# Kernel optimization log

Hardware: AMD Instinct MI355X
Metric: run time of the kernel (lower is better)

Reference implementation:

```python
import jax, jax.numpy as jnp
import numpy as np

N_HEADS, N_LEVELS, N_POINTS, D_MODEL = 8, 3, 12, 64
PARAM_NAMES = ['vp0_w','vp0_b','vp1_w','vp1_b','so0_w','so0_b','so1_w','so1_b','so2_w','so2_b','so3_w','so3_b','aw0_w','aw0_b','aw1_w','aw1_b','aw2_w','aw2_b','aw3_w','aw3_b','op0_w','op0_b','op1_w','op1_b']

def _lrelu(x):
    return jnp.where(x >= 0, x, 0.1 * x)

def _conv(x, w, b):
    y = jax.lax.conv_general_dilated(x, w, (1, 1), 'SAME', dimension_numbers=('NCHW', 'OIHW', 'NCHW'))
    return y + b[None, :, None, None]

def _bilinear(img, px, py):
    # img [B,C,H,W]; px,py [B,Q] absolute pixel coords; zero padding (grid_sample 'zeros')
    B, C, H, W = img.shape
    flat = img.reshape(B, C, H * W)
    x0 = jnp.floor(px); y0 = jnp.floor(py)
    wx1 = px - x0; wy1 = py - y0
    def g(xi, yi, wgt):
        valid = (xi >= 0) & (xi <= W - 1) & (yi >= 0) & (yi <= H - 1)
        xi_c = jnp.clip(xi, 0, W - 1).astype(jnp.int32)
        yi_c = jnp.clip(yi, 0, H - 1).astype(jnp.int32)
        v = jnp.take_along_axis(flat, (yi_c * W + xi_c)[:, None, :], axis=2)
        return v * (wgt * valid)[:, None, :]
    return (g(x0, y0, (1 - wx1) * (1 - wy1)) + g(x0 + 1, y0, wx1 * (1 - wy1))
          + g(x0, y0 + 1, (1 - wx1) * wy1) + g(x0 + 1, y0 + 1, wx1 * wy1))

def _flow_warp(img, flow):
    # img [n,C,h,w]; flow [n,2,h,w] (x,y); matches grid_sample align_corners=True
    n, C, h, w = img.shape
    gy, gx = jnp.meshgrid(jnp.arange(h, dtype=img.dtype), jnp.arange(w, dtype=img.dtype), indexing='ij')
    px = (gx[None] + flow[:, 0]).reshape(n, h * w)
    py = (gy[None] + flow[:, 1]).reshape(n, h * w)
    return _bilinear(img, px, py).reshape(n, C, h, w)

def _forward(x, flow_1, flow_2, flip_flow_1, flip_flow_2, p):
    n, t, c, h, w = x.shape
    hw = h * w; THW = t * hw
    M, L, P, D = N_HEADS, N_LEVELS, N_POINTS, c // N_HEADS
    flow_cn1 = flow_1
    flow_cn2 = flow_1 + _flow_warp(flow_2, flow_1)
    flow_n1c, flow_n1n2 = flip_flow_1, flow_2
    flow_n2n1 = flip_flow_2
    flow_n2c = flip_flow_2 + _flow_warp(flip_flow_1, flip_flow_2)
    warp_cn1 = _flow_warp(x[:, 1], flow_cn1)
    warp_cn2 = _flow_warp(x[:, 2], flow_cn2)
    warp_n1c = _flow_warp(x[:, 0], flow_n1c)
    warp_n1n2 = _flow_warp(x[:, 2], flow_n1n2)
    warp_n2n1 = _flow_warp(x[:, 1], flow_n2n1)
    warp_n2c = _flow_warp(x[:, 0], flow_n2c)
    extra = jnp.concatenate([x[:, 0], warp_cn1, warp_cn2, warp_n1c, warp_n1n2, warp_n2n1, warp_n2c,
                             flow_cn1, flow_cn2, flow_n1c, flow_n1n2, flow_n2n1, flow_n2c], axis=1)
    value = _conv(_lrelu(_conv(x.reshape(n, t * c, h, w), p['vp0_w'], p['vp0_b'])), p['vp1_w'], p['vp1_b'])
    def head(e, pre):
        y = _lrelu(_conv(e, p[pre + '0_w'], p[pre + '0_b']))
        y = _lrelu(_conv(y, p[pre + '1_w'], p[pre + '1_b']))
        y = _lrelu(_conv(y, p[pre + '2_w'], p[pre + '2_b']))
        return _conv(y, p[pre + '3_w'], p[pre + '3_b'])
    so = head(extra, 'so')  # [n, L*M*L*P*2, h, w]
    aw = head(extra, 'aw')  # [n, L*M*L*P*9, h, w]
    so = so.reshape(n, t, -1, hw).transpose(0, 1, 3, 2).reshape(n, THW, M, L, P, 2)
    aw = aw.reshape(n, t, -1, hw).transpose(0, 1, 3, 2).reshape(n, THW, M, L * P * 9)
    aw = jax.nn.softmax(aw, axis=-1).reshape(n, THW, M, L, P * 9)
    # flow-guided offsets: add per-(query-frame, target-level) flow to learned offsets
    off = so.reshape(n, t, hw, M, L, P, 2)
    fz = jnp.zeros_like(flow_cn2)
    def lvl(f0, f1, f2):
        s = jnp.stack([f0, f1, f2], 1)  # [n,3,2,h,w]
        return s.transpose(0, 3, 4, 1, 2).reshape(n, hw, L, 2)[:, None, :, None, :, None, :]
    off = jnp.concatenate([
        off[:, 0:1] + lvl(fz, flow_cn1, flow_cn2),
        off[:, 1:2] + lvl(flow_n1c, fz, flow_n1n2),
        off[:, 2:3] + lvl(flow_n2c, flow_n2n1, fz)], axis=1).reshape(n, THW, M, L, P, 2)
    # 3x3 integer patch around each sampling point
    pi, pj = jnp.meshgrid(jnp.arange(-1, 2), jnp.arange(-1, 2), indexing='ij')
    patch = jnp.stack([pi, pj], -1).reshape(1, 1, 1, 1, 1, 9, 2).astype(off.dtype)
    off = (off[..., None, :] + patch).reshape(n, THW, M, L, P * 9, 2)
    # reference points (valid_ratios are all 1: full masks are zeros)
    ry, rx = jnp.meshgrid((jnp.arange(h) + 0.5) / h, (jnp.arange(w) + 0.5) / w, indexing='ij')
    ref = jnp.stack([rx, ry], -1).reshape(1, hw, 2).astype(off.dtype)
    ref = jnp.tile(ref, (1, t, 1))  # [1, THW, 2]
    norm = jnp.array([w, h], dtype=off.dtype)
    loc = ref[:, :, None, None, None, :] + off / norm  # [n,THW,M,L,P*9,2] normalized
    # multi-scale deformable attention (all L levels share (h,w)); align_corners=False, zeros pad
    P9 = P * 9
    v = value.reshape(n, t, c, hw).transpose(0, 1, 3, 2).reshape(n, THW, M, D)
    vl = v.reshape(n, L, hw, M, D).transpose(0, 3, 1, 4, 2).reshape(n * M * L, D, h, w)
    px = (loc[..., 0] * w - 0.5).transpose(0, 2, 3, 1, 4).reshape(n * M * L, THW * P9)
    py = (loc[..., 1] * h - 0.5).transpose(0, 2, 3, 1, 4).reshape(n * M * L, THW * P9)
    sampled = _bilinear(vl, px, py).reshape(n, M, L, D, THW, P9)
    out = jnp.einsum('nmldqp,nqmlp->nqmd', sampled, aw).reshape(n, THW, c)
    out = out.reshape(n, t, h, w, c).transpose(0, 1, 4, 2, 3).reshape(n, t * c, h, w)
    out = _conv(_lrelu(_conv(out, p['op0_w'], p['op0_b'])), p['op1_w'], p['op1_b'])
    return out.reshape(n, t, c, h, w) + x

def setup_inputs():
    key = jax.random.key(0)
    n, t, c, h, w = 1, 3, 64, 32, 32
    ks = jax.random.split(key, 24)
    d = {}
    d['x'] = jax.random.normal(ks[0], (n, t, c, h, w), jnp.float32)
    for i, name in enumerate(['flow_1', 'flow_2', 'flip_flow_1', 'flip_flow_2']):
        d[name] = jax.random.normal(ks[1 + i], (n, 2, h, w), jnp.float32)
    cin_extra = 7 * c + 12
    specs = [('vp0', t * c, t * c), ('vp1', t * c, t * c),
             ('so0', c, cin_extra), ('so1', c, c), ('so2', c, c), ('so3', N_LEVELS * N_HEADS * N_LEVELS * N_POINTS * 2, c),
             ('aw0', c, cin_extra), ('aw1', c, c), ('aw2', c, c), ('aw3', N_LEVELS * N_HEADS * N_LEVELS * N_POINTS * 9, c),
             ('op0', t * c, t * c), ('op1', t * c, t * c)]
    for i, (name, co, ci) in enumerate(specs):
        kw, kb = jax.random.split(ks[5 + i])
        std = (2.0 / (ci * 9)) ** 0.5
        d[name + '_w'] = jax.random.normal(kw, (co, ci, 3, 3), jnp.float32) * std
        d[name + '_b'] = jax.random.normal(kb, (co,), jnp.float32) * 0.01
    return d

def reference(x, flow_1, flow_2, flip_flow_1, flip_flow_2, vp0_w, vp0_b, vp1_w, vp1_b, so0_w, so0_b, so1_w, so1_b, so2_w, so2_b, so3_w, so3_b, aw0_w, aw0_b, aw1_w, aw1_b, aw2_w, aw2_b, aw3_w, aw3_b, op0_w, op0_b, op1_w, op1_b):
    p = dict(zip(PARAM_NAMES, (vp0_w, vp0_b, vp1_w, vp1_b, so0_w, so0_b, so1_w, so1_b, so2_w, so2_b, so3_w, so3_b, aw0_w, aw0_b, aw1_w, aw1_b, aw2_w, aw2_b, aw3_w, aw3_b, op0_w, op0_b, op1_w, op1_b)))
    return _forward(x, flow_1, flow_2, flip_flow_1, flip_flow_2, p)
```

## Files before the change

### kernel.cpp

```cpp
#include <hip/hip_runtime.h>
#include <math.h>

#define HW 1024

typedef __attribute__((ext_vector_type(8))) short bf16x8;
typedef __attribute__((ext_vector_type(4))) float floatx4;

__device__ __forceinline__ unsigned short f2bf(float f) {
    unsigned u = __float_as_uint(f);
    u += 0x7FFF + ((u >> 16) & 1);
    return (unsigned short)(u >> 16);
}
__device__ __forceinline__ float bf2f(unsigned short u) {
    return __uint_as_float(((unsigned)u) << 16);
}
__device__ __forceinline__ float bflo(unsigned u) { return __uint_as_float(u << 16); }
__device__ __forceinline__ float bfhi(unsigned u) { return __uint_as_float(u & 0xffff0000u); }

__device__ __forceinline__ float bilin32(const float* __restrict__ img, float px, float py) {
    float x0f = floorf(px), y0f = floorf(py);
    float wx = px - x0f, wy = py - y0f;
    bool vx0 = (x0f >= 0.f) && (x0f <= 31.f);
    bool vx1 = (x0f >= -1.f) && (x0f <= 30.f);
    bool vy0 = (y0f >= 0.f) && (y0f <= 31.f);
    bool vy1 = (y0f >= -1.f) && (y0f <= 30.f);
    int ix0 = (int)fminf(fmaxf(x0f, 0.f), 31.f);
    int iy0 = (int)fminf(fmaxf(y0f, 0.f), 31.f);
    int ix1 = (int)fminf(fmaxf(x0f + 1.f, 0.f), 31.f);
    int iy1 = (int)fminf(fmaxf(y0f + 1.f, 0.f), 31.f);
    float w00 = (1.f - wx) * (1.f - wy) * ((vx0 && vy0) ? 1.f : 0.f);
    float w01 = wx * (1.f - wy) * ((vx1 && vy0) ? 1.f : 0.f);
    float w10 = (1.f - wx) * wy * ((vx0 && vy1) ? 1.f : 0.f);
    float w11 = wx * wy * ((vx1 && vy1) ? 1.f : 0.f);
    return w00 * img[iy0 * 32 + ix0] + w01 * img[iy0 * 32 + ix1] +
           w10 * img[iy1 * 32 + ix0] + w11 * img[iy1 * 32 + ix1];
}

__device__ __forceinline__ float2 comp_flow(const float* __restrict__ fa,
                                            const float* __restrict__ fb, int pix) {
    int y = pix >> 5, x = pix & 31;
    float fx = fa[pix], fy = fa[HW + pix];
    float px = (float)x + fx, py = (float)y + fy;
    float2 r;
    r.x = fx + bilin32(fb, px, py);
    r.y = fy + bilin32(fb + HW, px, py);
    return r;
}

struct WD { const float* src; int cout, Cin, nCb, wbase, beg; };
struct PrepP {
    const float *x, *f1, *f2, *ff1, *ff2;
    float *fcn2, *fn2c;
    unsigned short *x_pad, *extra_pad, *wgt;
    WD wd[12];
};

__global__ __launch_bounds__(256) void prep_k(PrepP P) {
    __shared__ float wlds[16 * 288];
    const int b = blockIdx.x, tid = threadIdx.x;
    if (b < 192) {
        int idx = b * 256 + tid;
        int pix = idx / 48, c4 = idx - pix * 48;
        int y = pix >> 5, xx = pix & 31;
        int c0 = c4 * 4;
        ushort4 s;
        s.x = f2bf(P.x[(size_t)(c0 + 0) * HW + pix]);
        s.y = f2bf(P.x[(size_t)(c0 + 1) * HW + pix]);
        s.z = f2bf(P.x[(size_t)(c0 + 2) * HW + pix]);
        s.w = f2bf(P.x[(size_t)(c0 + 3) * HW + pix]);
        *(ushort4*)(&P.x_pad[(size_t)((y + 1) * 34 + xx + 1) * 192 + c0]) = s;
    } else if (b < 2112) {
        int idx = (b - 192) * 256 + tid;
        int ch = idx >> 10, pix = idx & 1023;
        int y = pix >> 5, xx = pix & 31;
        float v = 0.f;
        if (ch < 64) {
            v = P.x[(size_t)ch * HW + pix];
        } else if (ch < 448) {
            int grp = (ch - 64) >> 6;
            int c = (ch - 64) & 63;
            const float* src;
            float fx, fy;
            if (grp == 0)      { src = P.x + 64 * HW;  fx = P.f1[pix];  fy = P.f1[HW + pix]; }
            else if (grp == 1) { src = P.x + 128 * HW; float2 r = comp_flow(P.f1, P.f2, pix);  fx = r.x; fy = r.y; }
            else if (grp == 2) { src = P.x;            fx = P.ff1[pix]; fy = P.ff1[HW + pix]; }
            else if (grp == 3) { src = P.x + 128 * HW; fx = P.f2[pix];  fy = P.f2[HW + pix]; }
            else if (grp == 4) { src = P.x + 64 * HW;  fx = P.ff2[pix]; fy = P.ff2[HW + pix]; }
            else               { src = P.x;            float2 r = comp_flow(P.ff2, P.ff1, pix); fx = r.x; fy = r.y; }
            v = bilin32(src + c * HW, (float)xx + fx, (float)y + fy);
        } else if (ch < 460) {
            int fc = ch - 448;
            int which = fc >> 1, comp = fc & 1;
            if (which == 0)      v = P.f1[comp * HW + pix];
            else if (which == 1) { float2 r = comp_flow(P.f1, P.f2, pix);  v = comp ? r.y : r.x; }
            else if (which == 2) v = P.ff1[comp * HW + pix];
            else if (which == 3) v = P.f2[comp * HW + pix];
            else if (which == 4) v = P.ff2[comp * HW + pix];
            else                 { float2 r = comp_flow(P.ff2, P.ff1, pix); v = comp ? r.y : r.x; }
        }
        P.extra_pad[(size_t)((y + 1) * 34 + xx + 1) * 480 + ch] = f2bf(v);
    } else if (b < 2128) {
        int idx = (b - 2112) * 256 + tid;
        if (idx < 1024) {
            float2 r = comp_flow(P.f1, P.f2, idx);
            P.fcn2[idx] = r.x; P.fcn2[HW + idx] = r.y;
        } else if (idx < 2048) {
            int pix = idx - 1024;
            float2 r = comp_flow(P.ff2, P.ff1, pix);
            P.fn2c[pix] = r.x; P.fn2c[HW + pix] = r.y;
        }
    } else if (b < 2144) {
        const int chans[9] = {192, 192, 480, 64, 64, 64, 64, 192, 192};
        size_t offs[9]; size_t a = 0;
        for (int i = 0; i < 9; ++i) { offs[i] = a; a += (size_t)1156 * chans[i]; }
        int bb = b - 2128;
        for (int item = bb; item < 9 * 132; item += 16) {
            int buf = item / 132, i = item - buf * 132;
            int py, px;
            if (i < 34) { py = 0; px = i; }
            else if (i < 68) { py = 33; px = i - 34; }
            else { int j = i - 68; py = 1 + (j >> 1); px = (j & 1) ? 33 : 0; }
            int C = chans[buf];
            unsigned short* p = P.x_pad + offs[buf] + (size_t)(py * 34 + px) * C;
            for (int c = tid; c < C; c += 256) p[c] = 0;
        }
    } else {
        int blk = b - 2144;
        int di = 0;
        while (di < 11 && blk >= P.wd[di + 1].beg) ++di;
        WD w = P.wd[di];
        int local = blk - w.beg;
        int co16 = local / w.nCb, cb = local - co16 * w.nCb;
        int cr0 = co16 * 16, ci0 = cb * 32;
        for (int i = tid; i < 16 * 288; i += 256) {
            int cr = i / 288, o = i - cr * 288;
            int crg = cr0 + cr, ci = ci0 + o / 9;
            float v = (crg < w.cout && ci < w.Cin)
                ? w.src[((size_t)crg * w.Cin + ci0) * 9 + o] : 0.f;
            wlds[i] = v;
        }
        __syncthreads();
        for (int e = tid; e < 9 * 512; e += 256) {
            int t = e >> 9, idx = e & 511;
            int j = idx & 7, lane = idx >> 3, q = lane >> 4, mm = lane & 15;
            P.wgt[((size_t)w.wbase + ((size_t)co16 * 9 + t) * w.nCb + cb) * 512 + idx] =
                f2bf(wlds[mm * 288 + (q * 8 + j) * 9 + t]);
        }
    }
}

struct CDesc {
    const unsigned short* in;
    const unsigned short* wgt;
    const float* bias;
    void* out;
    const float* residual;
    int Cpad, nCb, Cout, mode, cmod, relu, Mblocks;
};
struct CParam { CDesc d[4]; };

template<int PIXROWS, int COBLK>
__global__ __launch_bounds__(256) void conv_mfma_k(CParam P) {
    constexpr int TROWS = PIXROWS + 2;
    constexpr int TC = TROWS * 34 * 4;
    constexpr int ITRIPS = (TC + 255) / 256;
    constexpr int NTY = PIXROWS / 4;
    constexpr int NACC = NTY * 2;
    constexpr int MT = COBLK / 16;
    constexpr int WN = MT * 9 * 64;
    constexpr int WTRIPS = (WN + 255) / 256;
    __shared__ unsigned short blds[TROWS * 34 * 40];
    __shared__ unsigned short wlds[MT * 9 * 512];

    int bx = blockIdx.x;
    int di = 0;
    while (bx >= P.d[di].Mblocks) { bx -= P.d[di].Mblocks; ++di; }
    const CDesc d = P.d[di];

    const int tid = threadIdx.x;
    const int w = tid >> 6, lane = tid & 63;
    const int lq = lane >> 4, ln = lane & 15;
    const int co0 = bx * COBLK;
    const int by = blockIdx.y, y0 = by * PIXROWS;
    const unsigned short* __restrict__ in = d.in;
    const unsigned short* __restrict__ wg = d.wgt;
    const int Cpad = d.Cpad, nCb = d.nCb;

    floatx4 acc[MT][NACC];
#pragma unroll
    for (int mt = 0; mt < MT; ++mt)
#pragma unroll
        for (int nt = 0; nt < NACC; ++nt)
            acc[mt][nt] = (floatx4){0.f, 0.f, 0.f, 0.f};

    bf16x8 ireg[ITRIPS];
    bf16x8 wreg[WTRIPS];

    auto load_regs = [&](int cb) {
        const int ci0 = cb << 5;
#pragma unroll
        for (int k = 0; k < ITRIPS; ++k) {
            int i = tid + k * 256;
            if (i < TC) {
                int r = i / 136, rem = i - r * 136, c = rem >> 2, g = rem & 3;
                ireg[k] = *(const bf16x8*)(in + (size_t)((y0 + r) * 34 + c) * Cpad + ci0 + g * 8);
            }
        }
#pragma unroll
        for (int k = 0; k < WTRIPS; ++k) {
            int i = tid + k * 256;
            if (i < WN) {
                int chunk = i >> 6, l16 = i & 63;
                int mt = chunk / 9, t = chunk - mt * 9;
                wreg[k] = *(const bf16x8*)(wg + ((size_t)(((co0 >> 4) + mt) * 9 + t) * nCb + cb) * 512 + l16 * 8);
            }
        }
    };

    load_regs(0);

    for (int cb = 0; cb < nCb; ++cb) {
        __syncthreads();
#pragma unroll
        for (int k = 0; k < ITRIPS; ++k) {
            int i = tid + k * 256;
            if (i < TC) {
                int r = i / 136, rem = i - r * 136, c = rem >> 2, g = rem & 3;
                *(bf16x8*)(&blds[(r * 34 + c) * 40 + g * 8]) = ireg[k];
            }
        }
#pragma unroll
        for (int k = 0; k < WTRIPS; ++k) {
            int i = tid + k * 256;
            if (i < WN) {
                int chunk = i >> 6, l16 = i & 63;
                *(bf16x8*)(&wlds[chunk * 512 + l16 * 8]) = wreg[k];
            }
        }
        __syncthreads();
        if (cb + 1 < nCb) load_regs(cb + 1);
        for (int t = 0; t < 9; ++t) {
            const int dy = t / 3, dx = t - dy * 3;
            bf16x8 bfr[NACC];
#pragma unroll
            for (int ty = 0; ty < NTY; ++ty)
#pragma unroll
                for (int tx = 0; tx < 2; ++tx) {
                    int yy = w * NTY + ty + dy;
                    int xx = tx * 16 + ln + dx;
                    bfr[ty * 2 + tx] = *(const bf16x8*)(&blds[(yy * 34 + xx) * 40 + lq * 8]);
                }
#pragma unroll
            for (int mt = 0; mt < MT; ++mt) {
                bf16x8 afr = *(const bf16x8*)(&wlds[(mt * 9 + t) * 512 + lane * 8]);
#pragma unroll
                for (int nt = 0; nt < NACC; ++nt)
                    acc[mt][nt] = __builtin_amdgcn_mfma_f32_16x16x32_bf16(afr, bfr[nt], acc[mt][nt], 0, 0, 0);
            }
        }
    }

#pragma unroll
    for (int mt = 0; mt < MT; ++mt) {
        const int co = co0 + mt * 16 + lq * 4;
        if (co >= d.Cout) continue;
        float bv[4];
#pragma unroll
        for (int r = 0; r < 4; ++r) bv[r] = d.bias[co + r];
#pragma unroll
        for (int nt = 0; nt < NACC; ++nt) {
            const int ty = nt >> 1, tx = nt & 1;
            const int pix = by * (PIXROWS * 32) + (w * NTY + ty) * 32 + tx * 16 + ln;
            float v[4];
#pragma unroll
            for (int r = 0; r < 4; ++r) {
                float vv = acc[mt][nt][r] + bv[r];
                if (d.relu) vv = (vv >= 0.f) ? vv : 0.1f * vv;
                v[r] = vv;
            }
            if (d.mode == 0) {
                float* o = (float*)d.out;
#pragma unroll
                for (int r = 0; r < 4; ++r) {
                    float vv = v[r];
                    if (d.residual) vv += d.residual[(size_t)(co + r) * HW + pix];
                    o[(size_t)(co + r) * HW + pix] = vv;
                }
            } else if (d.mode == 1) {
                int fq = co / d.cmod, cc = co - fq * d.cmod;
                *(float4*)((float*)d.out + ((size_t)fq * HW + pix) * d.cmod + cc) =
                    make_float4(v[0], v[1], v[2], v[3]);
            } else if (d.mode == 2) {
                int fq = co / d.cmod, cc = co - fq * d.cmod;
                ushort4 s4;
                s4.x = f2bf(v[0]); s4.y = f2bf(v[1]); s4.z = f2bf(v[2]); s4.w = f2bf(v[3]);
                *(ushort4*)((unsigned short*)d.out + ((size_t)fq * HW + pix) * d.cmod + cc) = s4;
            } else {
                int yy = (pix >> 5) + 1, xx = (pix & 31) + 1;
                ushort4 s4;
                s4.x = f2bf(v[0]); s4.y = f2bf(v[1]); s4.z = f2bf(v[2]); s4.w = f2bf(v[3]);
                *(ushort4*)((unsigned short*)d.out + (size_t)(yy * 34 + xx) * d.cmod + co) = s4;
            }
        }
    }
}

__global__ __launch_bounds__(256) void deform_attn_k(
    const unsigned short* __restrict__ value_b, const float* __restrict__ so_t,
    const unsigned short* __restrict__ aw_t,
    const float* __restrict__ flow_1, const float* __restrict__ flow_2,
    const float* __restrict__ flip_flow_1, const float* __restrict__ flip_flow_2,
    const float* __restrict__ flow_cn2, const float* __restrict__ flow_n2c,
    unsigned short* __restrict__ attn_pad)
{
    __shared__ unsigned short vlds[24576];
    __shared__ unsigned short pwlds[4][432];
    const int tid = threadIdx.x;
    const int wav = tid >> 6, lane = tid & 63;
    const int m = blockIdx.x & 7, qc = blockIdx.x >> 3;

    for (int i = tid; i < 3072; i += 256) {
        int l = i >> 10, p = i & 1023;
        *(bf16x8*)(&vlds[(size_t)i * 8]) =
            *(const bf16x8*)(value_b + ((size_t)((l * 8 + m) * 1024) + p) * 8);
    }
    __syncthreads();

    const int pp = lane & 15, gq = lane >> 4;
    const int gdy = (gq >> 1) * 2 - 1;
    const int gdx = (gq & 1) * 2 - 1;
    const bool selx = (gq & 1);
    const bool sely = (gq >> 1);

    for (int r = 0; r < 8; ++r) {
        const int q = qc * 32 + r * 4 + wav;
        const int f = q >> 10, pix = q & 1023;
        const int y = pix >> 5, x = pix & 31;

        float flx0 = 0.f, fly0 = 0.f, flx1 = 0.f, fly1 = 0.f, flx2 = 0.f, fly2 = 0.f;
        if (f == 0) {
            flx1 = flow_1[pix];      fly1 = flow_1[HW + pix];
            flx2 = flow_cn2[pix];    fly2 = flow_cn2[HW + pix];
        } else if (f == 1) {
            flx0 = flip_flow_1[pix]; fly0 = flip_flow_1[HW + pix];
            flx2 = flow_2[pix];      fly2 = flow_2[HW + pix];
        } else {
            flx0 = flow_n2c[pix];    fly0 = flow_n2c[HW + pix];
            flx1 = flip_flow_2[pix]; fly1 = flip_flow_2[HW + pix];
        }

        const unsigned short* awp = aw_t + (size_t)q * 2592 + m * 324;
        float av[6];
        float vmax = -1e30f;
#pragma unroll
        for (int it = 0; it < 6; ++it) {
            int j = lane + it * 64;
            float a = (j < 324) ? bf2f(awp[j]) : -1e30f;
            av[it] = a;
            vmax = fmaxf(vmax, a);
        }
#pragma unroll
        for (int off = 32; off; off >>= 1) vmax = fmaxf(vmax, __shfl_xor(vmax, off));
        float ssum = 0.f;
#pragma unroll
        for (int it = 0; it < 6; ++it) {
            int j = lane + it * 64;
            float e = (j < 324) ? __expf(av[it] - vmax) : 0.f;
            av[it] = e;
            ssum += e;
        }
#pragma unroll
        for (int off = 32; off; off >>= 1) ssum += __shfl_xor(ssum, off);
        const float inv = 1.f / ssum;

#pragma unroll
        for (int it = 0; it < 6; ++it) {
            int j = lane + it * 64;
            if (j < 324) {
                int pi = j / 9, k = j - pi * 9;
                pwlds[wav][pi * 12 + k] = f2bf(av[it] * inv);
            }
        }

        float acc[8];
#pragma unroll
        for (int dd = 0; dd < 8; ++dd) acc[dd] = 0.f;
        const float* sop = so_t + (size_t)q * 576 + m * 72;

#pragma unroll
        for (int pt = 0; pt < 3; ++pt) {
            int pi = pt * 16 + pp;
            if (pi < 36) {
                int l = pi / 12;
                float2 so2 = *(const float2*)(sop + pi * 2);
                float fx = (l == 0) ? flx0 : (l == 1) ? flx1 : flx2;
                float fy = (l == 0) ? fly0 : (l == 1) ? fly1 : fly2;
                float bxf = (float)x + so2.x + fx;
                float byf = (float)y + so2.y + fy;
                float x0f = floorf(bxf), y0f = floorf(byf);
                float wx = bxf - x0f, wy = byf - y0f;
                float ax = 1.f - wx, ay = 1.f - wy;
                int x0 = (int)fminf(fmaxf(x0f, -2.f), 34.f);
                int y0 = (int)fminf(fmaxf(y0f, -2.f), 34.f);

                const unsigned short* pr = &pwlds[wav][pi * 12];
                uint2 pv0 = *(const uint2*)(pr);
                uint2 pv1 = *(const uint2*)(pr + 4);
                float a0 = bflo(pv0.x), a1 = bfhi(pv0.x), a2 = bflo(pv0.y);
                float a3 = bfhi(pv0.y), a4 = bflo(pv1.x), a5 = bfhi(pv1.x);
                float a6 = bflo(pv1.y), a7 = bfhi(pv1.y), a8 = bf2f(pr[8]);

                float bs0a, bs0b, bs1a, bs1b, bs2a, bs2b;
                {
                    float b0, b1, b2, b3;
                    b0 = a0 * ax; b1 = a0 * wx + a3 * ax; b2 = a3 * wx + a6 * ax; b3 = a6 * wx;
                    bs0a = selx ? b2 : b0; bs0b = selx ? b3 : b1;
                    b0 = a1 * ax; b1 = a1 * wx + a4 * ax; b2 = a4 * wx + a7 * ax; b3 = a7 * wx;
                    bs1a = selx ? b2 : b0; bs1b = selx ? b3 : b1;
                    b0 = a2 * ax; b1 = a2 * wx + a5 * ax; b2 = a5 * wx + a8 * ax; b3 = a8 * wx;
                    bs2a = selx ? b2 : b0; bs2b = selx ? b3 : b1;
                }
                float c00, c01, c10, c11;
                {
                    float c0 = bs0a * ay, c1 = bs0a * wy + bs1a * ay;
                    float c2 = bs1a * wy + bs2a * ay, c3 = bs2a * wy;
                    c00 = sely ? c2 : c0; c10 = sely ? c3 : c1;
                    c0 = bs0b * ay; c1 = bs0b * wy + bs1b * ay;
                    c2 = bs1b * wy + bs2b * ay; c3 = bs2b * wy;
                    c01 = sely ? c2 : c0; c11 = sely ? c3 : c1;
                }
                float cg[2][2] = {{c00, c01}, {c10, c11}};
                const int vbase = l * 1024;
#pragma unroll
                for (int sy = 0; sy < 2; ++sy) {
#pragma unroll
                    for (int sx = 0; sx < 2; ++sx) {
                        int dy = gdy + sy, dx = gdx + sx;
                        float pyf = y0f + (float)dy, pxf = x0f + (float)dx;
                        bool v = (pxf >= 0.f) && (pxf <= 31.f) && (pyf >= 0.f) && (pyf <= 31.f);
                        int px = min(max(x0 + dx, 0), 31);
                        int py = min(max(y0 + dy, 0), 31);
                        float c = cg[sy][sx] * (v ? 1.f : 0.f);
                        uint4 vv = *(const uint4*)(&vlds[(size_t)(vbase + py * 32 + px) * 8]);
                        acc[0] = fmaf(c, bflo(vv.x), acc[0]);
                        acc[1] = fmaf(c, bfhi(vv.x), acc[1]);
                        acc[2] = fmaf(c, bflo(vv.y), acc[2]);
                        acc[3] = fmaf(c, bfhi(vv.y), acc[3]);
                        acc[4] = fmaf(c, bflo(vv.z), acc[4]);
                        acc[5] = fmaf(c, bfhi(vv.z), acc[5]);
                        acc[6] = fmaf(c, bflo(vv.w), acc[6]);
                        acc[7] = fmaf(c, bfhi(vv.w), acc[7]);
                    }
                }
            }
        }

#pragma unroll
        for (int dd = 0; dd < 8; ++dd) {
#pragma unroll
            for (int off = 32; off; off >>= 1) acc[dd] += __shfl_xor(acc[dd], off);
        }
        if (lane == 0) {
            unsigned short* op = attn_pad + (size_t)((y + 1) * 34 + x + 1) * 192 + f * 64 + m * 8;
            ushort4 s0, s1;
            s0.x = f2bf(acc[0]); s0.y = f2bf(acc[1]); s0.z = f2bf(acc[2]); s0.w = f2bf(acc[3]);
            s1.x = f2bf(acc[4]); s1.y = f2bf(acc[5]); s1.z = f2bf(acc[6]); s1.w = f2bf(acc[7]);
            *(ushort4*)(op) = s0;
            *(ushort4*)(op + 4) = s1;
        }
    }
}

extern "C" void kernel_launch(void* const* d_in, const int* in_sizes, int n_in,
                              void* d_out, int out_size, void* d_ws, size_t ws_size,
                              hipStream_t stream) {
    const float* x      = (const float*)d_in[0];
    const float* flow_1 = (const float*)d_in[1];
    const float* flow_2 = (const float*)d_in[2];
    const float* flip_1 = (const float*)d_in[3];
    const float* flip_2 = (const float*)d_in[4];
    const float* vp0_w = (const float*)d_in[5];  const float* vp0_b = (const float*)d_in[6];
    const float* vp1_w = (const float*)d_in[7];  const float* vp1_b = (const float*)d_in[8];
    const float* so0_w = (const float*)d_in[9];  const float* so0_b = (const float*)d_in[10];
    const float* so1_w = (const float*)d_in[11]; const float* so1_b = (const float*)d_in[12];
    const float* so2_w = (const float*)d_in[13]; const float* so2_b = (const float*)d_in[14];
    const float* so3_w = (const float*)d_in[15]; const float* so3_b = (const float*)d_in[16];
    const float* aw0_w = (const float*)d_in[17]; const float* aw0_b = (const float*)d_in[18];
    const float* aw1_w = (const float*)d_in[19]; const float* aw1_b = (const float*)d_in[20];
    const float* aw2_w = (const float*)d_in[21]; const float* aw2_b = (const float*)d_in[22];
    const float* aw3_w = (const float*)d_in[23]; const float* aw3_b = (const float*)d_in[24];
    const float* op0_w = (const float*)d_in[25]; const float* op0_b = (const float*)d_in[26];
    const float* op1_w = (const float*)d_in[27]; const float* op1_b = (const float*)d_in[28];
    float* out = (float*)d_out;
    (void)ws_size; (void)in_sizes; (void)n_in; (void)out_size;

    float* fws = (float*)d_ws;
    float* flow_cn2 = fws;
    float* flow_n2c = flow_cn2 + 2048;
    unsigned short* value_b = (unsigned short*)(flow_n2c + 2048);
    float* so_t     = (float*)(value_b + 196608);
    unsigned short* uws = (unsigned short*)(so_t + 1769472);
    unsigned short* x_pad     = uws;
    unsigned short* vp0h      = x_pad + 1156 * 192;
    unsigned short* extra_pad = vp0h + 1156 * 192;
    unsigned short* s1 = extra_pad + 1156 * 480;
    unsigned short* a1 = s1 + 1156 * 64;
    unsigned short* s2 = a1 + 1156 * 64;
    unsigned short* a2 = s2 + 1156 * 64;
    unsigned short* attn_pad = a2 + 1156 * 64;
    unsigned short* op0h     = attn_pad + 1156 * 192;
    unsigned short* aw_t = op0h + 1156 * 192;
    unsigned short* wgt  = aw_t + (size_t)3072 * 2592;

    PrepP pp;
    pp.x = x; pp.f1 = flow_1; pp.f2 = flow_2; pp.ff1 = flip_1; pp.ff2 = flip_2;
    pp.fcn2 = flow_cn2; pp.fn2c = flow_n2c;
    pp.x_pad = x_pad; pp.extra_pad = extra_pad; pp.wgt = wgt;
    pp.wd[0]  = {vp0_w, 192, 192, 6,     0,    0};
    pp.wd[1]  = {vp1_w, 192, 192, 6,   648,   72};
    pp.wd[2]  = {so0_w,  64, 460, 15, 1296,  144};
    pp.wd[3]  = {aw0_w,  64, 460, 15, 1836,  204};
    pp.wd[4]  = {so1_w,  64,  64, 2,  2376,  264};
    pp.wd[5]  = {aw1_w,  64,  64, 2,  2448,  272};
    pp.wd[6]  = {so2_w,  64,  64, 2,  2520,  280};
    pp.wd[7]  = {aw2_w,  64,  64, 2,  2592,  288};
    pp.wd[8]  = {so3_w, 1728, 64, 2,  2664,  296};
    pp.wd[9]  = {aw3_w, 7776, 64, 2,  4608,  512};
    pp.wd[10] = {op0_w, 192, 192, 6, 13392, 1488};
    pp.wd[11] = {op1_w, 192, 192, 6, 14040, 1560};
    prep_k<<<3776, 256, 0, stream>>>(pp);

    const int BIG = 1 << 30;
    CDesc nul = {nullptr, nullptr, nullptr, nullptr, nullptr, 0, 0, 0, 0, 0, 0, BIG};

    {
        CParam cp;
        cp.d[0] = {x_pad,     wgt + (size_t)0 * 512,    vp0_b, vp0h, nullptr, 192, 6,  192, 3, 192, 1, 12};
        cp.d[1] = {extra_pad, wgt + (size_t)1296 * 512, so0_b, s1,   nullptr, 480, 15, 64,  3, 64,  1, 4};
        cp.d[2] = {extra_pad, wgt + (size_t)1836 * 512, aw0_b, a1,   nullptr, 480, 15, 64,  3, 64,  1, 4};
        cp.d[3] = nul;
        conv_mfma_k<4, 16><<<dim3(20, 8), 256, 0, stream>>>(cp);
    }
    {
        CParam cp;
        cp.d[0] = {vp0h, wgt + (size_t)648 * 512,  vp1_b, value_b, nullptr, 192, 6, 192, 2, 8,  0, 12};
        cp.d[1] = {s1,   wgt + (size_t)2376 * 512, so1_b, s2,      nullptr, 64,  2, 64,  3, 64, 1, 4};
        cp.d[2] = {a1,   wgt + (size_t)2448 * 512, aw1_b, a2,      nullptr, 64,  2, 64,  3, 64, 1, 4};
        cp.d[3] = nul;
        conv_mfma_k<4, 16><<<dim3(20, 8), 256, 0, stream>>>(cp);
    }
    {
        CParam cp;
        cp.d[0] = {s2, wgt + (size_t)2520 * 512, so2_b, s1, nullptr, 64, 2, 64, 3, 64, 1, 4};
        cp.d[1] = {a2, wgt + (size_t)2592 * 512, aw2_b, a1, nullptr, 64, 2, 64, 3, 64, 1, 4};
        cp.d[2] = nul; cp.d[3] = nul;
        conv_mfma_k<4, 16><<<dim3(8, 8), 256, 0, stream>>>(cp);
    }
    {
        CParam cp;
        cp.d[0] = {s1, wgt + (size_t)2664 * 512, so3_b, so_t, nullptr, 64, 2, 1728, 1, 576,  0, 27};
        cp.d[1] = {a1, wgt + (size_t)4608 * 512, aw3_b, aw_t, nullptr, 64, 2, 7776, 2, 2592, 0, 122};
        cp.d[2] = nul; cp.d[3] = nul;
        conv_mfma_k<8, 64><<<dim3(149, 4), 256, 0, stream>>>(cp);
    }

    deform_attn_k<<<768, 256, 0, stream>>>(value_b, so_t, aw_t,
                                           flow_1, flow_2, flip_1, flip_2,
                                           flow_cn2, flow_n2c, attn_pad);

    {
        CParam cp;
        cp.d[0] = {attn_pad, wgt + (size_t)13392 * 512, op0_b, op0h, nullptr, 192, 6, 192, 3, 192, 1, 12};
        cp.d[1] = nul; cp.d[2] = nul; cp.d[3] = nul;
        conv_mfma_k<4, 16><<<dim3(12, 8), 256, 0, stream>>>(cp);
    }
    {
        CParam cp;
        cp.d[0] = {op0h, wgt + (size_t)14040 * 512, op1_b, out, x, 192, 6, 192, 0, 0, 0, 12};
        cp.d[1] = nul; cp.d[2] = nul; cp.d[3] = nul;
        conv_mfma_k<4, 16><<<dim3(12, 8), 256, 0, stream>>>(cp);
    }
}
```

Before: 269.9 us.

## Spread weight transforms across conv launches and vectorize extra-channel prep

```diff
diff --git a/kernel.cpp b/kernel.cpp
--- a/kernel.cpp
+++ b/kernel.cpp
@@ -48,15 +48,38 @@
 }
 
 struct WD { const float* src; int cout, Cin, nCb, wbase, beg; };
+
+__device__ __forceinline__ void wxform_tile(const WD w, int local,
+                                            unsigned short* __restrict__ wgt, char* smraw) {
+    float* wlds = (float*)smraw;
+    const int tid = threadIdx.x;
+    int co16 = local / w.nCb, cb = local - co16 * w.nCb;
+    int cr0 = co16 * 16, ci0 = cb * 32;
+    for (int i = tid; i < 16 * 288; i += 256) {
+        int cr = i / 288, o = i - cr * 288;
+        int crg = cr0 + cr, ci = ci0 + o / 9;
+        float v = (crg < w.cout && ci < w.Cin)
+            ? w.src[((size_t)crg * w.Cin + ci0) * 9 + o] : 0.f;
+        wlds[i] = v;
+    }
+    __syncthreads();
+    for (int e = tid; e < 9 * 512; e += 256) {
+        int t = e >> 9, idx = e & 511;
+        int j = idx & 7, lane = idx >> 3, q = lane >> 4, mm = lane & 15;
+        wgt[((size_t)w.wbase + ((size_t)co16 * 9 + t) * w.nCb + cb) * 512 + idx] =
+            f2bf(wlds[mm * 288 + (q * 8 + j) * 9 + t]);
+    }
+}
+
 struct PrepP {
     const float *x, *f1, *f2, *ff1, *ff2;
     float *fcn2, *fn2c;
     unsigned short *x_pad, *extra_pad, *wgt;
-    WD wd[12];
+    WD wd[4];
 };
 
 __global__ __launch_bounds__(256) void prep_k(PrepP P) {
-    __shared__ float wlds[16 * 288];
+    __shared__ __align__(16) char sm[16 * 288 * 4];
     const int b = blockIdx.x, tid = threadIdx.x;
     if (b < 192) {
         int idx = b * 256 + tid;
@@ -69,38 +92,71 @@
         s.z = f2bf(P.x[(size_t)(c0 + 2) * HW + pix]);
         s.w = f2bf(P.x[(size_t)(c0 + 3) * HW + pix]);
         *(ushort4*)(&P.x_pad[(size_t)((y + 1) * 34 + xx + 1) * 192 + c0]) = s;
-    } else if (b < 2112) {
+    } else if (b < 672) {
         int idx = (b - 192) * 256 + tid;
-        int ch = idx >> 10, pix = idx & 1023;
+        int pix = idx / 120, c4 = idx - pix * 120;
         int y = pix >> 5, xx = pix & 31;
-        float v = 0.f;
-        if (ch < 64) {
-            v = P.x[(size_t)ch * HW + pix];
-        } else if (ch < 448) {
-            int grp = (ch - 64) >> 6;
-            int c = (ch - 64) & 63;
-            const float* src;
-            float fx, fy;
+        int c0 = c4 * 4;
+        float va[4];
+        if (c0 < 64) {
+#pragma unroll
+            for (int k = 0; k < 4; ++k) va[k] = P.x[(size_t)(c0 + k) * HW + pix];
+        } else if (c0 < 448) {
+            int grp = (c0 - 64) >> 6;
+            int c = (c0 - 64) & 63;
+            const float* src; float fx, fy;
             if (grp == 0)      { src = P.x + 64 * HW;  fx = P.f1[pix];  fy = P.f1[HW + pix]; }
             else if (grp == 1) { src = P.x + 128 * HW; float2 r = comp_flow(P.f1, P.f2, pix);  fx = r.x; fy = r.y; }
             else if (grp == 2) { src = P.x;            fx = P.ff1[pix]; fy = P.ff1[HW + pix]; }
             else if (grp == 3) { src = P.x + 128 * HW; fx = P.f2[pix];  fy = P.f2[HW + pix]; }
             else if (grp == 4) { src = P.x + 64 * HW;  fx = P.ff2[pix]; fy = P.ff2[HW + pix]; }
             else               { src = P.x;            float2 r = comp_flow(P.ff2, P.ff1, pix); fx = r.x; fy = r.y; }
-            v = bilin32(src + c * HW, (float)xx + fx, (float)y + fy);
-        } else if (ch < 460) {
-            int fc = ch - 448;
-            int which = fc >> 1, comp = fc & 1;
-            if (which == 0)      v = P.f1[comp * HW + pix];
-            else if (which == 1) { float2 r = comp_flow(P.f1, P.f2, pix);  v = comp ? r.y : r.x; }
-            else if (which == 2) v = P.ff1[comp * HW + pix];
-            else if (which == 3) v = P.f2[comp * HW + pix];
-            else if (which == 4) v = P.ff2[comp * HW + pix];
-            else                 { float2 r = comp_flow(P.ff2, P.ff1, pix); v = comp ? r.y : r.x; }
-        }
-        P.extra_pad[(size_t)((y + 1) * 34 + xx + 1) * 480 + ch] = f2bf(v);
-    } else if (b < 2128) {
-        int idx = (b - 2112) * 256 + tid;
+            float px = (float)xx + fx, py = (float)y + fy;
+            float x0f = floorf(px), y0f = floorf(py);
+            float wx = px - x0f, wy = py - y0f;
+            bool vx0 = (x0f >= 0.f) && (x0f <= 31.f);
+            bool vx1 = (x0f >= -1.f) && (x0f <= 30.f);
+            bool vy0 = (y0f >= 0.f) && (y0f <= 31.f);
+            bool vy1 = (y0f >= -1.f) && (y0f <= 30.f);
+            int ix0 = (int)fminf(fmaxf(x0f, 0.f), 31.f);
+            int iy0 = (int)fminf(fmaxf(y0f, 0.f), 31.f);
+            int ix1 = (int)fminf(fmaxf(x0f + 1.f, 0.f), 31.f);
+            int iy1 = (int)fminf(fmaxf(y0f + 1.f, 0.f), 31.f);
+            float w00 = (1.f - wx) * (1.f - wy) * ((vx0 && vy0) ? 1.f : 0.f);
+            float w01 = wx * (1.f - wy) * ((vx1 && vy0) ? 1.f : 0.f);
+            float w10 = (1.f - wx) * wy * ((vx0 && vy1) ? 1.f : 0.f);
+            float w11 = wx * wy * ((vx1 && vy1) ? 1.f : 0.f);
+            int p00 = iy0 * 32 + ix0, p01 = iy0 * 32 + ix1;
+            int p10 = iy1 * 32 + ix0, p11 = iy1 * 32 + ix1;
+            const float* im = src + (size_t)c * HW;
+#pragma unroll
+            for (int k = 0; k < 4; ++k) {
+                va[k] = w00 * im[p00] + w01 * im[p01] + w10 * im[p10] + w11 * im[p11];
+                im += HW;
+            }
+        } else {
+#pragma unroll
+            for (int k = 0; k < 4; ++k) {
+                int ch = c0 + k;
+                float v = 0.f;
+                if (ch < 460) {
+                    int fc = ch - 448;
+                    int which = fc >> 1, comp = fc & 1;
+                    if (which == 0)      v = P.f1[comp * HW + pix];
+                    else if (which == 1) { float2 r = comp_flow(P.f1, P.f2, pix);  v = comp ? r.y : r.x; }
+                    else if (which == 2) v = P.ff1[comp * HW + pix];
+                    else if (which == 3) v = P.f2[comp * HW + pix];
+                    else if (which == 4) v = P.ff2[comp * HW + pix];
+                    else                 { float2 r = comp_flow(P.ff2, P.ff1, pix); v = comp ? r.y : r.x; }
+                }
+                va[k] = v;
+            }
+        }
+        ushort4 s;
+        s.x = f2bf(va[0]); s.y = f2bf(va[1]); s.z = f2bf(va[2]); s.w = f2bf(va[3]);
+        *(ushort4*)(&P.extra_pad[(size_t)((y + 1) * 34 + xx + 1) * 480 + c0]) = s;
+    } else if (b < 688) {
+        int idx = (b - 672) * 256 + tid;
         if (idx < 1024) {
             float2 r = comp_flow(P.f1, P.f2, idx);
             P.fcn2[idx] = r.x; P.fcn2[HW + idx] = r.y;
@@ -109,11 +165,11 @@
             float2 r = comp_flow(P.ff2, P.ff1, pix);
             P.fn2c[pix] = r.x; P.fn2c[HW + pix] = r.y;
         }
-    } else if (b < 2144) {
+    } else if (b < 704) {
         const int chans[9] = {192, 192, 480, 64, 64, 64, 64, 192, 192};
         size_t offs[9]; size_t a = 0;
         for (int i = 0; i < 9; ++i) { offs[i] = a; a += (size_t)1156 * chans[i]; }
-        int bb = b - 2128;
+        int bb = b - 688;
         for (int item = bb; item < 9 * 132; item += 16) {
             int buf = item / 132, i = item - buf * 132;
             int py, px;
@@ -125,27 +181,10 @@
             for (int c = tid; c < C; c += 256) p[c] = 0;
         }
     } else {
-        int blk = b - 2144;
+        int blk = b - 704;
         int di = 0;
-        while (di < 11 && blk >= P.wd[di + 1].beg) ++di;
-        WD w = P.wd[di];
-        int local = blk - w.beg;
-        int co16 = local / w.nCb, cb = local - co16 * w.nCb;
-        int cr0 = co16 * 16, ci0 = cb * 32;
-        for (int i = tid; i < 16 * 288; i += 256) {
-            int cr = i / 288, o = i - cr * 288;
-            int crg = cr0 + cr, ci = ci0 + o / 9;
-            float v = (crg < w.cout && ci < w.Cin)
-                ? w.src[((size_t)crg * w.Cin + ci0) * 9 + o] : 0.f;
-            wlds[i] = v;
-        }
-        __syncthreads();
-        for (int e = tid; e < 9 * 512; e += 256) {
-            int t = e >> 9, idx = e & 511;
-            int j = idx & 7, lane = idx >> 3, q = lane >> 4, mm = lane & 15;
-            P.wgt[((size_t)w.wbase + ((size_t)co16 * 9 + t) * w.nCb + cb) * 512 + idx] =
-                f2bf(wlds[mm * 288 + (q * 8 + j) * 9 + t]);
-        }
+        while (di < 3 && blk >= P.wd[di + 1].beg) ++di;
+        wxform_tile(P.wd[di], blk - P.wd[di].beg, P.wgt, sm);
     }
 }
 
@@ -157,10 +196,17 @@
     const float* residual;
     int Cpad, nCb, Cout, mode, cmod, relu, Mblocks;
 };
-struct CParam { CDesc d[4]; };
+struct CParam {
+    CDesc d[4];
+    WD rwd[4];
+    int rbeg[5];
+    int nr;
+    int ride_bx0;
+    unsigned short* wgt;
+};
 
 template<int PIXROWS, int COBLK>
-__global__ __launch_bounds__(256) void conv_mfma_k(CParam P) {
+__device__ __forceinline__ void conv_tile(const CDesc d, int bx, int by, char* smraw) {
     constexpr int TROWS = PIXROWS + 2;
     constexpr int TC = TROWS * 34 * 4;
     constexpr int ITRIPS = (TC + 255) / 256;
@@ -169,19 +215,14 @@
     constexpr int MT = COBLK / 16;
     constexpr int WN = MT * 9 * 64;
     constexpr int WTRIPS = (WN + 255) / 256;
-    __shared__ unsigned short blds[TROWS * 34 * 40];
-    __shared__ unsigned short wlds[MT * 9 * 512];
-
-    int bx = blockIdx.x;
-    int di = 0;
-    while (bx >= P.d[di].Mblocks) { bx -= P.d[di].Mblocks; ++di; }
-    const CDesc d = P.d[di];
+    unsigned short* blds = (unsigned short*)smraw;
+    unsigned short* wlds = (unsigned short*)(smraw + TROWS * 34 * 40 * 2);
 
     const int tid = threadIdx.x;
     const int w = tid >> 6, lane = tid & 63;
     const int lq = lane >> 4, ln = lane & 15;
     const int co0 = bx * COBLK;
-    const int by = blockIdx.y, y0 = by * PIXROWS;
+    const int y0 = by * PIXROWS;
     const unsigned short* __restrict__ in = d.in;
     const unsigned short* __restrict__ wg = d.wgt;
     const int Cpad = d.Cpad, nCb = d.nCb;
@@ -305,6 +346,26 @@
     }
 }
 
+template<int PIXROWS, int COBLK>
+__global__ __launch_bounds__(256) void conv_mfma_k(CParam P) {
+    constexpr int TROWS = PIXROWS + 2;
+    constexpr int MT = COBLK / 16;
+    constexpr int SMB = TROWS * 34 * 40 * 2 + MT * 9 * 512 * 2;
+    __shared__ __align__(16) char sm[(SMB > 18432) ? SMB : 18432];
+    int bx = blockIdx.x;
+    if (P.nr > 0 && bx >= P.ride_bx0) {
+        int slot = (bx - P.ride_bx0) * gridDim.y + blockIdx.y;
+        if (slot >= P.rbeg[P.nr]) return;
+        int di = 0;
+        while (di + 1 < P.nr && slot >= P.rbeg[di + 1]) ++di;
+        wxform_tile(P.rwd[di], slot - P.rbeg[di], P.wgt, sm);
+        return;
+    }
+    int di = 0;
+    while (bx >= P.d[di].Mblocks) { bx -= P.d[di].Mblocks; ++di; }
+    conv_tile<PIXROWS, COBLK>(P.d[di], bx, blockIdx.y, sm);
+}
+
 __global__ __launch_bounds__(256) void deform_attn_k(
     const unsigned short* __restrict__ value_b, const float* __restrict__ so_t,
     const unsigned short* __restrict__ aw_t,
@@ -332,10 +393,29 @@
     const bool selx = (gq & 1);
     const bool sely = (gq >> 1);
 
+    float av[6];
+    {
+        const unsigned short* awp = aw_t + (size_t)(qc * 32 + wav) * 2592 + m * 324;
+#pragma unroll
+        for (int it = 0; it < 6; ++it) {
+            int j = lane + it * 64;
+            av[it] = (j < 324) ? bf2f(awp[j]) : -1e30f;
+        }
+    }
+
     for (int r = 0; r < 8; ++r) {
         const int q = qc * 32 + r * 4 + wav;
         const int f = q >> 10, pix = q & 1023;
         const int y = pix >> 5, x = pix & 31;
+
+        const float* sop = so_t + (size_t)q * 576 + m * 72;
+        float2 so2r[3];
+#pragma unroll
+        for (int pt = 0; pt < 3; ++pt) {
+            int pi = pt * 16 + pp;
+            if (pi < 36) so2r[pt] = *(const float2*)(sop + pi * 2);
+            else { so2r[pt].x = 0.f; so2r[pt].y = 0.f; }
+        }
 
         float flx0 = 0.f, fly0 = 0.f, flx1 = 0.f, fly1 = 0.f, flx2 = 0.f, fly2 = 0.f;
         if (f == 0) {
@@ -349,16 +429,9 @@
             flx1 = flip_flow_2[pix]; fly1 = flip_flow_2[HW + pix];
         }
 
-        const unsigned short* awp = aw_t + (size_t)q * 2592 + m * 324;
-        float av[6];
         float vmax = -1e30f;
 #pragma unroll
-        for (int it = 0; it < 6; ++it) {
-            int j = lane + it * 64;
-            float a = (j < 324) ? bf2f(awp[j]) : -1e30f;
-            av[it] = a;
-            vmax = fmaxf(vmax, a);
-        }
+        for (int it = 0; it < 6; ++it) vmax = fmaxf(vmax, av[it]);
 #pragma unroll
         for (int off = 32; off; off >>= 1) vmax = fmaxf(vmax, __shfl_xor(vmax, off));
         float ssum = 0.f;
@@ -382,17 +455,26 @@
             }
         }
 
+        float avn[6];
+        if (r < 7) {
+            const unsigned short* awn = aw_t + (size_t)(q + 4) * 2592 + m * 324;
+#pragma unroll
+            for (int it = 0; it < 6; ++it) {
+                int j = lane + it * 64;
+                avn[it] = (j < 324) ? bf2f(awn[j]) : -1e30f;
+            }
+        }
+
         float acc[8];
 #pragma unroll
         for (int dd = 0; dd < 8; ++dd) acc[dd] = 0.f;
-        const float* sop = so_t + (size_t)q * 576 + m * 72;
 
 #pragma unroll
         for (int pt = 0; pt < 3; ++pt) {
             int pi = pt * 16 + pp;
             if (pi < 36) {
                 int l = pi / 12;
-                float2 so2 = *(const float2*)(sop + pi * 2);
+                float2 so2 = so2r[pt];
                 float fx = (l == 0) ? flx0 : (l == 1) ? flx1 : flx2;
                 float fy = (l == 0) ? fly0 : (l == 1) ? fly1 : fly2;
                 float bxf = (float)x + so2.x + fx;
@@ -467,6 +549,10 @@
             s1.x = f2bf(acc[4]); s1.y = f2bf(acc[5]); s1.z = f2bf(acc[6]); s1.w = f2bf(acc[7]);
             *(ushort4*)(op) = s0;
             *(ushort4*)(op + 4) = s1;
+        }
+        if (r < 7) {
+#pragma unroll
+            for (int it = 0; it < 6; ++it) av[it] = avn[it];
         }
     }
 }
@@ -516,22 +602,15 @@
     pp.x = x; pp.f1 = flow_1; pp.f2 = flow_2; pp.ff1 = flip_1; pp.ff2 = flip_2;
     pp.fcn2 = flow_cn2; pp.fn2c = flow_n2c;
     pp.x_pad = x_pad; pp.extra_pad = extra_pad; pp.wgt = wgt;
-    pp.wd[0]  = {vp0_w, 192, 192, 6,     0,    0};
-    pp.wd[1]  = {vp1_w, 192, 192, 6,   648,   72};
-    pp.wd[2]  = {so0_w,  64, 460, 15, 1296,  144};
-    pp.wd[3]  = {aw0_w,  64, 460, 15, 1836,  204};
-    pp.wd[4]  = {so1_w,  64,  64, 2,  2376,  264};
-    pp.wd[5]  = {aw1_w,  64,  64, 2,  2448,  272};
-    pp.wd[6]  = {so2_w,  64,  64, 2,  2520,  280};
-    pp.wd[7]  = {aw2_w,  64,  64, 2,  2592,  288};
-    pp.wd[8]  = {so3_w, 1728, 64, 2,  2664,  296};
-    pp.wd[9]  = {aw3_w, 7776, 64, 2,  4608,  512};
-    pp.wd[10] = {op0_w, 192, 192, 6, 13392, 1488};
-    pp.wd[11] = {op1_w, 192, 192, 6, 14040, 1560};
-    prep_k<<<3776, 256, 0, stream>>>(pp);
+    pp.wd[0] = {vp0_w, 192, 192, 6,     0,   0};
+    pp.wd[1] = {vp1_w, 192, 192, 6,   648,  72};
+    pp.wd[2] = {so0_w,  64, 460, 15, 1296, 144};
+    pp.wd[3] = {aw0_w,  64, 460, 15, 1836, 204};
+    prep_k<<<968, 256, 0, stream>>>(pp);
 
     const int BIG = 1 << 30;
     CDesc nul = {nullptr, nullptr, nullptr, nullptr, nullptr, 0, 0, 0, 0, 0, 0, BIG};
+    WD wnul = {nullptr, 0, 0, 1, 0, 0};
 
     {
         CParam cp;
@@ -539,7 +618,13 @@
         cp.d[1] = {extra_pad, wgt + (size_t)1296 * 512, so0_b, s1,   nullptr, 480, 15, 64,  3, 64,  1, 4};
         cp.d[2] = {extra_pad, wgt + (size_t)1836 * 512, aw0_b, a1,   nullptr, 480, 15, 64,  3, 64,  1, 4};
         cp.d[3] = nul;
-        conv_mfma_k<4, 16><<<dim3(20, 8), 256, 0, stream>>>(cp);
+        cp.rwd[0] = {so1_w, 64, 64, 2, 2376, 0};
+        cp.rwd[1] = {aw1_w, 64, 64, 2, 2448, 0};
+        cp.rwd[2] = {so2_w, 64, 64, 2, 2520, 0};
+        cp.rwd[3] = {aw2_w, 64, 64, 2, 2592, 0};
+        cp.rbeg[0] = 0; cp.rbeg[1] = 8; cp.rbeg[2] = 16; cp.rbeg[3] = 24; cp.rbeg[4] = 32;
+        cp.nr = 4; cp.ride_bx0 = 20; cp.wgt = wgt;
+        conv_mfma_k<4, 16><<<dim3(24, 8), 256, 0, stream>>>(cp);
     }
     {
         CParam cp;
@@ -547,20 +632,33 @@
         cp.d[1] = {s1,   wgt + (size_t)2376 * 512, so1_b, s2,      nullptr, 64,  2, 64,  3, 64, 1, 4};
         cp.d[2] = {a1,   wgt + (size_t)2448 * 512, aw1_b, a2,      nullptr, 64,  2, 64,  3, 64, 1, 4};
         cp.d[3] = nul;
-        conv_mfma_k<4, 16><<<dim3(20, 8), 256, 0, stream>>>(cp);
+        cp.rwd[0] = {so3_w, 1728, 64, 2, 2664, 0};
+        cp.rwd[1] = {aw3_w, 7776, 64, 2, 4608, 0};
+        cp.rwd[2] = wnul; cp.rwd[3] = wnul;
+        cp.rbeg[0] = 0; cp.rbeg[1] = 216; cp.rbeg[2] = 1188; cp.rbeg[3] = 1188; cp.rbeg[4] = 1188;
+        cp.nr = 2; cp.ride_bx0 = 20; cp.wgt = wgt;
+        conv_mfma_k<4, 16><<<dim3(169, 8), 256, 0, stream>>>(cp);
     }
     {
         CParam cp;
         cp.d[0] = {s2, wgt + (size_t)2520 * 512, so2_b, s1, nullptr, 64, 2, 64, 3, 64, 1, 4};
         cp.d[1] = {a2, wgt + (size_t)2592 * 512, aw2_b, a1, nullptr, 64, 2, 64, 3, 64, 1, 4};
         cp.d[2] = nul; cp.d[3] = nul;
-        conv_mfma_k<4, 16><<<dim3(8, 8), 256, 0, stream>>>(cp);
+        cp.rwd[0] = {op0_w, 192, 192, 6, 13392, 0};
+        cp.rwd[1] = {op1_w, 192, 192, 6, 14040, 0};
+        cp.rwd[2] = wnul; cp.rwd[3] = wnul;
+        cp.rbeg[0] = 0; cp.rbeg[1] = 72; cp.rbeg[2] = 144; cp.rbeg[3] = 144; cp.rbeg[4] = 144;
+        cp.nr = 2; cp.ride_bx0 = 8; cp.wgt = wgt;
+        conv_mfma_k<4, 16><<<dim3(26, 8), 256, 0, stream>>>(cp);
     }
     {
         CParam cp;
         cp.d[0] = {s1, wgt + (size_t)2664 * 512, so3_b, so_t, nullptr, 64, 2, 1728, 1, 576,  0, 27};
         cp.d[1] = {a1, wgt + (size_t)4608 * 512, aw3_b, aw_t, nullptr, 64, 2, 7776, 2, 2592, 0, 122};
         cp.d[2] = nul; cp.d[3] = nul;
+        cp.nr = 0; cp.ride_bx0 = BIG; cp.wgt = wgt;
+        cp.rwd[0] = wnul; cp.rwd[1] = wnul; cp.rwd[2] = wnul; cp.rwd[3] = wnul;
+        cp.rbeg[0] = 0; cp.rbeg[1] = 0; cp.rbeg[2] = 0; cp.rbeg[3] = 0; cp.rbeg[4] = 0;
         conv_mfma_k<8, 64><<<dim3(149, 4), 256, 0, stream>>>(cp);
     }
 
@@ -572,12 +670,18 @@
         CParam cp;
         cp.d[0] = {attn_pad, wgt + (size_t)13392 * 512, op0_b, op0h, nullptr, 192, 6, 192, 3, 192, 1, 12};
         cp.d[1] = nul; cp.d[2] = nul; cp.d[3] = nul;
+        cp.nr = 0; cp.ride_bx0 = BIG; cp.wgt = wgt;
+        cp.rwd[0] = wnul; cp.rwd[1] = wnul; cp.rwd[2] = wnul; cp.rwd[3] = wnul;
+        cp.rbeg[0] = 0; cp.rbeg[1] = 0; cp.rbeg[2] = 0; cp.rbeg[3] = 0; cp.rbeg[4] = 0;
         conv_mfma_k<4, 16><<<dim3(12, 8), 256, 0, stream>>>(cp);
     }
     {
         CParam cp;
         cp.d[0] = {op0h, wgt + (size_t)14040 * 512, op1_b, out, x, 192, 6, 192, 0, 0, 0, 12};
         cp.d[1] = nul; cp.d[2] = nul; cp.d[3] = nul;
+        cp.nr = 0; cp.ride_bx0 = BIG; cp.wgt = wgt;
+        cp.rwd[0] = wnul; cp.rwd[1] = wnul; cp.rwd[2] = wnul; cp.rwd[3] = wnul;
+        cp.rbeg[0] = 0; cp.rbeg[1] = 0; cp.rbeg[2] = 0; cp.rbeg[3] = 0; cp.rbeg[4] = 0;
         conv_mfma_k<4, 16><<<dim3(12, 8), 256, 0, stream>>>(cp);
     }
 }
```

New measurement: 281.9 us. 1.04x slower.
